# Performance work log

Hardware: AMD Instinct MI355X
Metric: run time of the kernel (lower is better)

## Reference

```python
import jax, jax.numpy as jnp
import numpy as np

B, S, D = 8192, 8, 96

def setup_inputs() -> dict:
    key = jax.random.key(0)
    ks = jax.random.split(key, 6)
    x = jax.random.normal(ks[0], (B, 1, S, D), dtype=jnp.float32)
    # nn.Linear(8,8): weight (8,8), bias (8,)
    Wp = jax.random.normal(ks[1], (S, S), dtype=jnp.float32) * (1.0 / np.sqrt(S))
    bp = jax.random.normal(ks[2], (S,), dtype=jnp.float32) * 0.02
    # three nn.Linear(96,96, bias=False): weight (96,96)
    sc = 1.0 / np.sqrt(D)
    Wv = jax.random.normal(ks[3], (D, D), dtype=jnp.float32) * sc
    Wk = jax.random.normal(ks[4], (D, D), dtype=jnp.float32) * sc
    Wq = jax.random.normal(ks[5], (D, D), dtype=jnp.float32) * sc
    return {"x": x, "Wp": Wp, "bp": bp, "Wv": Wv, "Wk": Wk, "Wq": Wq}

def reference(x, Wp, bp, Wv, Wk, Wq):
    # x: (B,1,S,D) -> squeeze(1) -> (B,S,D)
    h = jnp.squeeze(x, axis=1)
    p = jnp.arange(S, dtype=jnp.float32)
    # nn.Linear on a 1-D vector: p @ Wp.T + bp -> (S,), then view(S,1)
    pos = (p @ Wp.T + bp)[:, None]            # (S,1)
    embed = h + pos                            # broadcast over D
    values = embed @ Wv.T                      # (B,S,D)
    keys = embed @ Wk.T
    queries = embed @ Wq.T
    # einsum 'bqx,bky->bxy' contracts q and k independently (outer product of seq-sums)
    scores = jnp.einsum('bqx,bky->bxy', queries, keys)   # (B,D,D)
    attention = jax.nn.softmax(scores, axis=1)           # softmax over x (dim=1)
    # einsum 'bxy,bvn->bvy' sums attention over x and values over n
    out = jnp.einsum('bxy,bvn->bvy', attention, values)  # (B,S,D)
    return out
```

## Files before the change

### kernel.cpp

```cpp
#include <hip/hip_runtime.h>
#include <hip/hip_bf16.h>


#define NTHR 1024
#define NBLK 512

__global__ __launch_bounds__(NTHR) void attn_fused_kernel(
    const float* __restrict__ x, const float* __restrict__ Wp,
    const float* __restrict__ bp, const float* __restrict__ Wv,
    float* __restrict__ out) {
    __shared__ __align__(16) float4 part[32][24];
    __shared__ __align__(16) float4 col4[24];
    __shared__ float posv[8];

    const int t = threadIdx.x;
    const int c = blockIdx.x * NTHR + t;
    const int row = c >> 3, sub = c & 7;

    const float* xb = x + (size_t)row * 96 + sub * 4;
    float4 a0 = *(const float4*)(xb);
    float4 a1 = *(const float4*)(xb + 32);
    float4 a2 = *(const float4*)(xb + 64);

    const float4* Wv4 = (const float4*)Wv;
    if (t < 768) {
        const int slot = t % 24;
        const int g    = t / 24;
        const int n0   = g * 3;
        float4 s0 = Wv4[(n0 + 0) * 24 + slot];
        float4 s1 = Wv4[(n0 + 1) * 24 + slot];
        float4 s2 = Wv4[(n0 + 2) * 24 + slot];
        part[g][slot] = make_float4(s0.x + s1.x + s2.x, s0.y + s1.y + s2.y,
                                    s0.z + s1.z + s2.z, s0.w + s1.w + s2.w);
    } else if (t < 776) {
        const int s = t - 768;
        float p = bp[s];
        #pragma unroll
        for (int j = 1; j < 8; ++j) p += (float)j * Wp[s * 8 + j];
        posv[s] = p;
    }
    __syncthreads();
    if (t < 24) {
        float4 cc = part[0][t];
        #pragma unroll
        for (int g = 1; g < 32; ++g) {
            float4 q = part[g][t];
            cc.x += q.x; cc.y += q.y; cc.z += q.z; cc.w += q.w;
        }
        col4[t] = cc;
    }
    __syncthreads();

    float4 w0 = col4[sub + 0], w1 = col4[sub + 8], w2 = col4[sub + 16];
    const float p = posv[row & 7];
    float dot = (a0.x + p) * w0.x + (a0.y + p) * w0.y + (a0.z + p) * w0.z + (a0.w + p) * w0.w
              + (a1.x + p) * w1.x + (a1.y + p) * w1.y + (a1.z + p) * w1.z + (a1.w + p) * w1.w
              + (a2.x + p) * w2.x + (a2.y + p) * w2.y + (a2.z + p) * w2.z + (a2.w + p) * w2.w;
    dot += __shfl_xor(dot, 1);
    dot += __shfl_xor(dot, 2);
    dot += __shfl_xor(dot, 4);
    float4 v = make_float4(dot, dot, dot, dot);
    float* ob = out + (size_t)row * 96 + sub * 4;
    *(float4*)(ob)      = v;
    *(float4*)(ob + 32) = v;
    *(float4*)(ob + 64) = v;
}

extern "C" void kernel_launch(void* const* d_in, const int* in_sizes, int n_in,
                              void* d_out, int out_size, void* d_ws, size_t ws_size,
                              hipStream_t stream) {
    const float* x  = (const float*)d_in[0];
    const float* Wp = (const float*)d_in[1];
    const float* bp = (const float*)d_in[2];
    const float* Wv = (const float*)d_in[3];
    float* out = (float*)d_out;

    attn_fused_kernel<<<NBLK, NTHR, 0, stream>>>(x, Wp, bp, Wv, out);
}
```

Before: 14.56 us.

## Split weight-column reduction into a one-block setup kernel before streaming kernel

Moves the per-block reduction of Wv column sums and the position term into a single-block setup kernel that writes 96 column sums and 8 per-row additive constants to workspace. The streaming kernel then only loads those from workspace and computes a plain dot product plus a row constant, with smaller 256-thread blocks. This removes 512 redundant recomputations of the 96x96 Wv reduction, at the cost of an extra kernel launch and a serial dependency between the two launches.

```diff
diff --git a/kernel.cpp b/kernel.cpp
--- a/kernel.cpp
+++ b/kernel.cpp
@@ -2,26 +2,17 @@
 #include <hip/hip_bf16.h>
 
 
-#define NTHR 1024
-#define NBLK 512
+#define NTHR_B 256
+#define NBLK_B 2048
 
-__global__ __launch_bounds__(NTHR) void attn_fused_kernel(
-    const float* __restrict__ x, const float* __restrict__ Wp,
-    const float* __restrict__ bp, const float* __restrict__ Wv,
-    float* __restrict__ out) {
+__global__ __launch_bounds__(1024) void setup_kernel(
+    const float* __restrict__ Wp, const float* __restrict__ bp,
+    const float* __restrict__ Wv, float* __restrict__ ws) {
     __shared__ __align__(16) float4 part[32][24];
-    __shared__ __align__(16) float4 col4[24];
+    __shared__ __align__(16) float4 cols[24];
     __shared__ float posv[8];
 
     const int t = threadIdx.x;
-    const int c = blockIdx.x * NTHR + t;
-    const int row = c >> 3, sub = c & 7;
-
-    const float* xb = x + (size_t)row * 96 + sub * 4;
-    float4 a0 = *(const float4*)(xb);
-    float4 a1 = *(const float4*)(xb + 32);
-    float4 a2 = *(const float4*)(xb + 64);
-
     const float4* Wv4 = (const float4*)Wv;
     if (t < 768) {
         const int slot = t % 24;
@@ -41,25 +32,55 @@
     }
     __syncthreads();
     if (t < 24) {
-        float4 cc = part[0][t];
+        float4 c = part[0][t];
         #pragma unroll
         for (int g = 1; g < 32; ++g) {
             float4 q = part[g][t];
-            cc.x += q.x; cc.y += q.y; cc.z += q.z; cc.w += q.w;
+            c.x += q.x; c.y += q.y; c.z += q.z; c.w += q.w;
         }
-        col4[t] = cc;
+        cols[t] = c;
+        ((float4*)ws)[t] = c;
     }
+    __syncthreads();
+    if (t < 8) {
+        float W = 0.f;
+        #pragma unroll
+        for (int k = 0; k < 24; ++k) {
+            float4 c = cols[k];
+            W += c.x + c.y + c.z + c.w;
+        }
+        ws[96 + t] = posv[t] * W;
+    }
+}
+
+__global__ __launch_bounds__(NTHR_B) void stream_kernel(
+    const float* __restrict__ x, const float* __restrict__ ws,
+    float* __restrict__ out) {
+    __shared__ __align__(16) float4 col4[24];
+    __shared__ float rowadd[8];
+
+    const int t = threadIdx.x;
+    const int c = blockIdx.x * NTHR_B + t;
+    const int row = c >> 3, sub = c & 7;
+
+    const float* xb = x + (size_t)row * 96 + sub * 4;
+    float4 a0 = *(const float4*)(xb);
+    float4 a1 = *(const float4*)(xb + 32);
+    float4 a2 = *(const float4*)(xb + 64);
+
+    if (t < 24) col4[t] = ((const float4*)ws)[t];
+    else if (t >= 32 && t < 40) rowadd[t - 32] = ws[96 + (t - 32)];
     __syncthreads();
 
     float4 w0 = col4[sub + 0], w1 = col4[sub + 8], w2 = col4[sub + 16];
-    const float p = posv[row & 7];
-    float dot = (a0.x + p) * w0.x + (a0.y + p) * w0.y + (a0.z + p) * w0.z + (a0.w + p) * w0.w
-              + (a1.x + p) * w1.x + (a1.y + p) * w1.y + (a1.z + p) * w1.z + (a1.w + p) * w1.w
-              + (a2.x + p) * w2.x + (a2.y + p) * w2.y + (a2.z + p) * w2.z + (a2.w + p) * w2.w;
+    float dot = a0.x * w0.x + a0.y * w0.y + a0.z * w0.z + a0.w * w0.w
+              + a1.x * w1.x + a1.y * w1.y + a1.z * w1.z + a1.w * w1.w
+              + a2.x * w2.x + a2.y * w2.y + a2.z * w2.z + a2.w * w2.w;
     dot += __shfl_xor(dot, 1);
     dot += __shfl_xor(dot, 2);
     dot += __shfl_xor(dot, 4);
-    float4 v = make_float4(dot, dot, dot, dot);
+    const float val = dot + rowadd[row & 7];
+    float4 v = make_float4(val, val, val, val);
     float* ob = out + (size_t)row * 96 + sub * 4;
     *(float4*)(ob)      = v;
     *(float4*)(ob + 32) = v;
@@ -74,6 +95,8 @@
     const float* bp = (const float*)d_in[2];
     const float* Wv = (const float*)d_in[3];
     float* out = (float*)d_out;
+    float* ws  = (float*)d_ws;
 
-    attn_fused_kernel<<<NBLK, NTHR, 0, stream>>>(x, Wp, bp, Wv, out);
+    setup_kernel<<<1, 1024, 0, stream>>>(Wp, bp, Wv, ws);
+    stream_kernel<<<NBLK_B, NTHR_B, 0, stream>>>(x, ws, out);
 }
```

Result: slower. 17.70 us (+21.6%).
